# Optimization experiments

Hardware: AMD Instinct MI355X
Metric: run time of the kernel (lower is better)

## Reference

```python
import jax, jax.numpy as jnp
import numpy as np

# Config (matches init_kwargs): range [-32,32]^3, voxel 0.5 -> 128^3 grid; BEV 200x200
PC_LOW = np.array([-32.0, -32.0, -32.0], dtype=np.float32)
PC_HIGH = np.array([32.0, 32.0, 32.0], dtype=np.float32)
VOX = 0.5
G = 128
BEV_H, BEV_W = 200, 200
BN_EPS = 1e-5
STRIDES = [1, 2, 1, 2, 1, 1]


def setup_inputs() -> dict:
    key = jax.random.key(0)
    ks = jax.random.split(key, 10)
    N = 2_000_000
    xyz = jax.random.uniform(ks[0], (N, 3), jnp.float32, minval=-32.0, maxval=32.0)
    inten = jax.random.uniform(ks[1], (N, 1), jnp.float32)
    points = jnp.concatenate([xyz, inten], axis=1)  # (N,4)
    chans = [(32, 4), (64, 32), (64, 64), (128, 64), (128, 128), (256, 128)]
    inp = {"points": points}
    for i, (co, ci) in enumerate(chans):
        fan_in = ci * 27
        inp[f"w{i+1}"] = jax.random.normal(ks[2 + i], (co, ci, 3, 3, 3), jnp.float32) / np.sqrt(fan_in)
        inp[f"g{i+1}"] = jnp.ones((co,), jnp.float32)
        inp[f"b{i+1}"] = jnp.zeros((co,), jnp.float32)
    return inp


def _voxelize(points):
    # range filtering + floor-binning + clamp, faithful to voxelize_points (dense path: scatter-ADD)
    low = jnp.asarray(PC_LOW)
    high = jnp.asarray(PC_HIGH)
    mask = jnp.all((points[:, :3] >= low) & (points[:, :3] <= high), axis=1)
    coords = jnp.floor((points[:, :3] - low) / VOX).astype(jnp.int32)
    coords = jnp.clip(coords, 0, G - 1)
    vals = points * mask[:, None].astype(points.dtype)  # invalid points contribute 0
    # original indexes voxel_grid[:, z, y, x]
    grid = jnp.zeros((G, G, G, 4), points.dtype)
    grid = grid.at[coords[:, 2], coords[:, 1], coords[:, 0]].add(vals)
    return jnp.transpose(grid, (3, 0, 1, 2))  # (4, G, G, G)


def _conv3d(x, w, s):
    # PyTorch Conv3d(k=3, padding=1, stride=s), NCDHW
    return jax.lax.conv_general_dilated(
        x, w, window_strides=(s, s, s), padding=[(1, 1), (1, 1), (1, 1)],
        dimension_numbers=("NCDHW", "OIDHW", "NCDHW"))


def _bn_relu(x, g, b):
    # eval-mode BN: running_mean=0, running_var=1
    scale = (g / jnp.sqrt(1.0 + BN_EPS))[None, :, None, None, None]
    return jax.nn.relu(x * scale + b[None, :, None, None, None])


def reference(points, w1, w2, w3, w4, w5, w6,
              g1, g2, g3, g4, g5, g6,
              b1, b2, b3, b4, b5, b6):
    ws = [w1, w2, w3, w4, w5, w6]
    gs = [g1, g2, g3, g4, g5, g6]
    bs = [b1, b2, b3, b4, b5, b6]
    x = _voxelize(points)[None]  # (1,4,G,G,G)
    for w, g, b, s in zip(ws, gs, bs, STRIDES):
        x = _bn_relu(_conv3d(x, w, s), g, b)
    feat = x[0]  # (256, G/4, G/4, G/4)
    bev = jnp.max(feat, axis=2)  # torch.max(..., dim=2) on (C,D1,D2,D3) -> (C,D1,D3)
    # F.interpolate bilinear align_corners=False == jax.image.resize half-pixel bilinear
    bev = jax.image.resize(bev, (bev.shape[0], BEV_H, BEV_W), method="bilinear")
    return bev
```

## Files before the change

kernel.cpp:

```cpp
#include <hip/hip_runtime.h>
#include <hip/hip_fp16.h>
#include <cstdint>
#include <cstddef>

typedef __attribute__((ext_vector_type(8))) short short8;
typedef __attribute__((ext_vector_type(8))) _Float16 half8;
typedef __attribute__((ext_vector_type(16))) float f32x16;

__device__ __forceinline__ float bf2f(unsigned short u) { return __uint_as_float(((unsigned)u) << 16); }
__device__ __forceinline__ unsigned short f2bf(float f) {
    unsigned u = __float_as_uint(f);
    return (unsigned short)((u + 0x7fffu + ((u >> 16) & 1u)) >> 16);
}
__device__ __forceinline__ void sync_lds() {
    asm volatile("s_waitcnt lgkmcnt(0)\n\ts_barrier" ::: "memory");
}
__device__ __forceinline__ void sync_vm() {
    asm volatile("s_waitcnt vmcnt(0)\n\ts_barrier" ::: "memory");
}
__device__ __forceinline__ void gload16(const unsigned short* g, char* l) {
    __builtin_amdgcn_global_load_lds(
        (const __attribute__((address_space(1))) unsigned int*)g,
        (__attribute__((address_space(3))) unsigned int*)l, 16, 0, 0);
}

static constexpr float BN_INV = 0.9999950000374997f;


__device__ __forceinline__ int vox_bucket(float4 p, bool& ok) {
    ok = !(p.x < -32.f || p.x > 32.f || p.y < -32.f || p.y > 32.f || p.z < -32.f || p.z > 32.f);
    int cy = min(max((int)floorf((p.y + 32.f) * 2.f), 0), 127);
    int cz = min(max((int)floorf((p.z + 32.f) * 2.f), 0), 127);
    return cz * 4 + (cy >> 5);
}

__global__ __launch_bounds__(256) void vox_count(const float4* __restrict__ pts,
                                                 int* __restrict__ cnt, int N) {
    __shared__ int h[512];
    for (int t = threadIdx.x; t < 512; t += 256) h[t] = 0;
    __syncthreads();
    int stride = gridDim.x * 256;
    for (int i = blockIdx.x * 256 + threadIdx.x; i < N; i += stride) {
        float4 p = pts[i];
        bool ok;
        int bk = vox_bucket(p, ok);
        if (ok) atomicAdd(&h[bk], 1);
    }
    __syncthreads();
    for (int t = threadIdx.x; t < 512; t += 256)
        if (h[t]) atomicAdd(&cnt[t], h[t]);
}

__global__ void vox_scan(const int* __restrict__ cnt, int* __restrict__ off,
                         int* __restrict__ cur) {
    __shared__ int c[512];
    int t = threadIdx.x;
    c[t] = cnt[t];
    __syncthreads();
    int s = 0;
    for (int i = 0; i < t; ++i) s += c[i];
    off[t] = s;
    cur[t] = s;
}

__global__ __launch_bounds__(256) void vox_scatter(const float4* __restrict__ pts,
                                                   int* __restrict__ cur,
                                                   float4* __restrict__ sorted, int N) {
    __shared__ int h[512];
    __shared__ int base[512];
    int b0 = blockIdx.x * 4096;
    for (int t = threadIdx.x; t < 512; t += 256) h[t] = 0;
    __syncthreads();
    float4 p[16];
    int bk[16];
#pragma unroll
    for (int j = 0; j < 16; ++j) {
        int i = b0 + j * 256 + threadIdx.x;
        bk[j] = -1;
        if (i < N) {
            p[j] = pts[i];
            bool ok;
            int b = vox_bucket(p[j], ok);
            if (ok) {
                bk[j] = b;
                atomicAdd(&h[b], 1);
            }
        }
    }
    __syncthreads();
    for (int t = threadIdx.x; t < 512; t += 256) {
        int n = h[t];
        base[t] = n ? atomicAdd(&cur[t], n) : 0;
        h[t] = 0;
    }
    __syncthreads();
#pragma unroll
    for (int j = 0; j < 16; ++j) {
        if (bk[j] >= 0) {
            int r = atomicAdd(&h[bk[j]], 1);
            sorted[base[bk[j]] + r] = p[j];
        }
    }
}

__global__ __launch_bounds__(256) void vox_accum(const float4* __restrict__ sorted,
                                                 const int* __restrict__ off,
                                                 const int* __restrict__ cnt,
                                                 __half2* __restrict__ grid) {
    __shared__ float s[32 * 128 * 4];
    for (int t = threadIdx.x; t < 16384; t += 256) s[t] = 0.f;
    __syncthreads();
    int bid = blockIdx.x;
    int bz = bid >> 2;
    int ylo = (bid & 3) << 5;
    int b = off[bid], n = cnt[bid];
    for (int i = threadIdx.x; i < n; i += 256) {
        float4 p = sorted[b + i];
        int cx = min(max((int)floorf((p.x + 32.f) * 2.f), 0), 127);
        int cy = min(max((int)floorf((p.y + 32.f) * 2.f), 0), 127);
        float* v = s + ((cy - ylo) * 128 + cx) * 4;
        unsafeAtomicAdd(v + 0, p.x);
        unsafeAtomicAdd(v + 1, p.y);
        unsafeAtomicAdd(v + 2, p.z);
        unsafeAtomicAdd(v + 3, p.w);
    }
    __syncthreads();
    for (int t = threadIdx.x; t < 4096; t += 256) {
        int ry = t >> 7, cx = t & 127;
        const float* v = s + t * 4;
        union { __half2 h[2]; float2 f; } u;
        u.h[0] = __floats2half2_rn(v[0], v[1]);
        u.h[1] = __floats2half2_rn(v[2], v[3]);
        int gi = (((bz + 1) * 130 + (ylo + ry + 1)) * 130 + (cx + 1)) * 2;
        *(float2*)(grid + gi) = u.f;
    }
}

__global__ __launch_bounds__(256) void pad_zero(unsigned short* __restrict__ buf,
                                                int Xp, int Zp, int C) {
    const int cpc = (C >= 8) ? (C / 8) : 1;
    long i = (long)blockIdx.x * 256 + threadIdx.x;
    long nz = (long)2 * Xp * Xp;
    long ny = (long)(Zp - 2) * 2 * Xp;
    long nx = (long)(Zp - 2) * (Xp - 2) * 2;
    long total = (nz + ny + nx) * cpc;
    if (i >= total) return;
    long cell = i / cpc;
    int ch = (int)(i - cell * cpc) * 8;
    int z, y, x;
    if (cell < nz) {
        long r = cell;
        z = (r >= (long)Xp * Xp) ? (Zp - 1) : 0;
        r %= (long)Xp * Xp;
        y = (int)(r / Xp);
        x = (int)(r % Xp);
    } else if (cell < nz + ny) {
        long r = cell - nz;
        z = 1 + (int)(r / (2 * Xp));
        int s = (int)(r % (2 * Xp));
        y = (s >= Xp) ? (Xp - 1) : 0;
        x = (s >= Xp) ? (s - Xp) : s;
    } else {
        long r = cell - nz - ny;
        z = 1 + (int)(r / ((Xp - 2) * 2));
        int s = (int)(r % ((Xp - 2) * 2));
        y = 1 + (s >> 1);
        x = (s & 1) ? (Xp - 1) : 0;
    }
    unsigned short* p = buf + (((long)z * Xp + y) * Xp + x) * C + ch;
    if (C >= 8) {
        *(short8*)p = (short8){0, 0, 0, 0, 0, 0, 0, 0};
    } else {
        *(float2*)p = (float2){0.f, 0.f};
    }
}
static inline int pad_blocks(int Xp, int Zp, int C) {
    long cells = (long)2 * Xp * Xp + (long)(Zp - 2) * 2 * Xp + (long)(Zp - 2) * (Xp - 2) * 2;
    long thr = cells * ((C >= 8) ? (C / 8) : 1);
    return (int)((thr + 255) / 256);
}

__global__ __launch_bounds__(256) void repack_w(const float* __restrict__ w, const float* __restrict__ g,
                                                unsigned short* __restrict__ o, int Co, int CI) {
    int i = blockIdx.x * 256 + threadIdx.x;
    int total = 27 * Co * CI;
    if (i >= total) return;
    int ci = i % CI;
    int t = i / CI;
    int co = t % Co;
    int k = t / Co;
    float v = w[((size_t)(co * CI + ci)) * 27 + k] * g[co] * BN_INV;
    o[i] = f2bf(v);
}
__global__ __launch_bounds__(256) void repack_w1m(const float* __restrict__ w, const float* __restrict__ g,
                                                  unsigned short* __restrict__ o) {
    int i = blockIdx.x * 256 + threadIdx.x;
    if (i >= 9 * 32 * 16) return;
    int k16 = i & 15;
    int co = (i >> 4) & 31;
    int p = i >> 9;
    float v = 0.f;
    if (k16 < 12) {
        int dx = k16 >> 2, ci = k16 & 3;
        int dz = p / 3, dy = p % 3;
        v = w[(co * 4 + ci) * 27 + dz * 9 + dy * 3 + dx] * g[co] * BN_INV;
    }
    o[i] = __half_as_ushort(__float2half(v));
}

__global__ __launch_bounds__(256) void conv1_mfma(
    const unsigned short* __restrict__ in, const unsigned short* __restrict__ wa,
    const float* __restrict__ beta, unsigned short* __restrict__ out,
    int zstart, int r0) {
    const int tid = threadIdx.x;
    const int l31 = tid & 31;
    const int lh = (tid >> 5) & 1;
    const int wv = tid >> 6;
    int v = blockIdx.x * 128 + wv * 32 + l31;
    int x = v & 127;
    int y = (v >> 7) & 127;
    int z = zstart + (v >> 14);

    const unsigned short* base = in + ((z * 130 + y) * 130 + x) * 4 + lh * 8;
    uint2 d0[9], d1[9];
    half8 a[9];
#pragma unroll
    for (int p = 0; p < 9; ++p) {
        int dz = p / 3, dy = p % 3;
        const unsigned short* rp = base + (dz * 130 + dy) * 520;
        d0[p] = *(const uint2*)(rp);
        d1[p] = *(const uint2*)(rp + 4);
        a[p] = *(const half8*)(wa + (p * 32 + l31) * 16 + lh * 8);
    }
    f32x16 acc = {0.f};
#pragma unroll
    for (int p = 0; p < 9; ++p) {
        uint4 braw = {d0[p].x, d0[p].y, d1[p].x, d1[p].y};
        half8 b = *(half8*)&braw;
        acc = __builtin_amdgcn_mfma_f32_32x32x16_f16(a[p], b, acc, 0, 0, 0);
    }
    int r = z - zstart + r0;
    int ob = ((r * 130 + (y + 1)) * 130 + (x + 1)) * 32;
#pragma unroll
    for (int g = 0; g < 4; ++g) {
        int cb = 4 * lh + 8 * g;
        float4 bt = *(const float4*)(beta + cb);
        ushort4 u;
        u.x = f2bf(fmaxf(acc[g * 4 + 0] + bt.x, 0.f));
        u.y = f2bf(fmaxf(acc[g * 4 + 1] + bt.y, 0.f));
        u.z = f2bf(fmaxf(acc[g * 4 + 2] + bt.z, 0.f));
        u.w = f2bf(fmaxf(acc[g * 4 + 3] + bt.w, 0.f));
        *(ushort4*)(out + ob + cb) = u;
    }
}

template <int CI, int KC, int S>
__global__ __launch_bounds__(256) void conv_mfma(
    const unsigned short* __restrict__ in, const unsigned short* __restrict__ wb,
    const float* __restrict__ beta, unsigned short* __restrict__ out,
    int D, int lgD, int Xp, int Xpo, int Co, int zin_base, int v_off) {

    constexpr int KCp = KC + 8;
    constexpr int OPB = KC / 8;
    constexpr int NB = KC / 16;
    constexpr int NA = KC / 32;
    constexpr int NCH = KC / 16;
    constexpr int NCC = CI / KC;
    constexpr int STOT = 27 * NCC;

    __shared__ __align__(16) short sA[2 * 64 * KCp];
    __shared__ __align__(16) short sB[2 * 128 * KCp];

    const int tid = threadIdx.x;
    const int l31 = tid & 31;
    const int lh = (tid >> 5) & 1;
    const int wv = tid >> 6;

    const unsigned gx = gridDim.x;
    const unsigned lin = blockIdx.y * gx + blockIdx.x;
    const unsigned q = (gx * gridDim.y) >> 3;
    const unsigned lin2 = (lin & 7) * q + (lin >> 3);
    const unsigned bxs = lin2 % gx;
    const unsigned bys = lin2 / gx;
    const int co0 = bxs * 64;

    int bgIdx[NB], blB[NB];
#pragma unroll
    for (int j = 0; j < NB; ++j) {
        int idx = tid + j * 256;
        int vL = idx / OPB;
        int oct = idx - vL * OPB;
        int vg = v_off + bys * 128 + vL;
        int x = vg & (D - 1);
        int ry = vg >> lgD;
        int y = ry & (D - 1);
        int z = ry >> lgD;
        bgIdx[j] = ((z * S * Xp + y * S) * Xp + x * S) * CI + oct * 8;
        blB[j] = vL * KCp + oct * 8;
    }
    int agIdx[NA], alA[NA];
#pragma unroll
    for (int j = 0; j < NA; ++j) {
        int idx = tid + j * 256;
        int cA = idx / OPB;
        int oct = idx - cA * OPB;
        agIdx[j] = (co0 + cA) * CI + oct * 8;
        alA[j] = cA * KCp + oct * 8;
    }
    const int bfr = (wv * 32 + l31) * KCp + lh * 8;
    const int afr = l31 * KCp + lh * 8;

    short8 rB[2][NB], rA[2][NA];

    auto loadStage = [&](int s, int r) {
        int k = s / NCC;
        int c0 = (s - k * NCC) * KC;
        int dz = k / 9;
        int rr = k - dz * 9;
        int dy = rr / 3;
        int dx = rr - dy * 3;
        int kb = (((dz - zin_base) * Xp + dy) * Xp + dx) * CI + c0;
        int ka = k * Co * CI + c0;
#pragma unroll
        for (int j = 0; j < NB; ++j) rB[r][j] = *(const short8*)(in + bgIdx[j] + kb);
#pragma unroll
        for (int j = 0; j < NA; ++j) rA[r][j] = *(const short8*)(wb + agIdx[j] + ka);
    };
    auto storeLDS = [&](int r, int buf) {
#pragma unroll
        for (int j = 0; j < NB; ++j) *(short8*)(sB + buf * 128 * KCp + blB[j]) = rB[r][j];
#pragma unroll
        for (int j = 0; j < NA; ++j) *(short8*)(sA + buf * 64 * KCp + alA[j]) = rA[r][j];
    };

    f32x16 acc0 = {0.f}, acc1 = {0.f};

    loadStage(0, 0);
    loadStage(1, 1);
    storeLDS(0, 0);
    sync_lds();

#pragma unroll
    for (int s = 0; s < STOT; ++s) {
        if (s + 2 < STOT) loadStage(s + 2, s & 1);
        const short* pB = sB + (s & 1) * 128 * KCp + bfr;
        const short* pA = sA + (s & 1) * 64 * KCp + afr;
#pragma unroll
        for (int c = 0; c < NCH; ++c) {
            short8 bv = *(const short8*)(pB + c * 16);
            short8 a0 = *(const short8*)(pA + c * 16);
            short8 a1 = *(const short8*)(pA + 32 * KCp + c * 16);
            acc0 = __builtin_amdgcn_mfma_f32_32x32x16_bf16(a0, bv, acc0, 0, 0, 0);
            acc1 = __builtin_amdgcn_mfma_f32_32x32x16_bf16(a1, bv, acc1, 0, 0, 0);
        }
        if (s + 1 < STOT) {
            storeLDS((s + 1) & 1, (s + 1) & 1);
            sync_lds();
        }
    }

    int vg = v_off + bys * 128 + wv * 32 + l31;
    int x = vg & (D - 1);
    int ry = vg >> lgD;
    int y = ry & (D - 1);
    int z = ry >> lgD;
    size_t ob = (((size_t)(z + 1) * Xpo + (y + 1)) * Xpo + (x + 1)) * Co + co0;
#pragma unroll
    for (int cot = 0; cot < 2; ++cot) {
        const f32x16& a = cot ? acc1 : acc0;
#pragma unroll
        for (int g = 0; g < 4; ++g) {
            int cb = cot * 32 + 4 * lh + 8 * g;
            float4 bt = *(const float4*)(beta + co0 + cb);
            ushort4 u;
            u.x = f2bf(fmaxf(a[g * 4 + 0] + bt.x, 0.f));
            u.y = f2bf(fmaxf(a[g * 4 + 1] + bt.y, 0.f));
            u.z = f2bf(fmaxf(a[g * 4 + 2] + bt.z, 0.f));
            u.w = f2bf(fmaxf(a[g * 4 + 3] + bt.w, 0.f));
            *(ushort4*)(out + ob + cb) = u;
        }
    }
}

template <int CI, int S>
__global__ __launch_bounds__(256, 3) void conv_mfma_g(
    const unsigned short* __restrict__ in, const unsigned short* __restrict__ wb,
    const float* __restrict__ beta, unsigned short* __restrict__ out,
    int D, int lgD, int Xp, int Xpo, int Co, int zin_base, int v_off) {

    constexpr int KC = 64;
    constexpr int NCC = CI / KC;
    constexpr int STOT = 27 * NCC;

    __shared__ __align__(16) char sB[2 * 128 * 128];
    __shared__ __align__(16) char sA[2 * 64 * 128];

    const int tid = threadIdx.x;
    const int l31 = tid & 31;
    const int lh = (tid >> 5) & 1;
    const int wv = tid >> 6;
    const int l63 = tid & 63;

    const unsigned gx = gridDim.x;
    const unsigned lin = blockIdx.y * gx + blockIdx.x;
    const unsigned q = (gx * gridDim.y) >> 3;
    const unsigned lin2 = (lin & 7) * q + (lin >> 3);
    const unsigned bxs = lin2 % gx;
    const unsigned bys = lin2 / gx;
    const int co0 = bxs * 64;

    const int swoct = (l63 & 7) ^ (l63 >> 3);

    int bgIdxG[4];
#pragma unroll
    for (int j = 0; j < 4; ++j) {
        int r = (j * 4 + wv) * 8 + (l63 >> 3);
        int vg = v_off + bys * 128 + r;
        int x = vg & (D - 1);
        int ry = vg >> lgD;
        int y = ry & (D - 1);
        int z = ry >> lgD;
        bgIdxG[j] = ((z * S * Xp + y * S) * Xp + x * S) * CI + swoct * 8;
    }
    int agIdxG[2];
#pragma unroll
    for (int j = 0; j < 2; ++j) {
        int r = (j * 4 + wv) * 8 + (l63 >> 3);
        agIdxG[j] = (co0 + r) * CI + swoct * 8;
    }

    auto issueStage = [&](int s, int buf) {
        int k = s / NCC;
        int c0 = (s - k * NCC) * KC;
        int dz = k / 9;
        int rr = k - dz * 9;
        int dy = rr / 3;
        int dx = rr - dy * 3;
        int kb = (((dz - zin_base) * Xp + dy) * Xp + dx) * CI + c0;
        int ka = k * Co * CI + c0;
#pragma unroll
        for (int j = 0; j < 4; ++j)
            gload16(in + bgIdxG[j] + kb, sB + buf * 16384 + (j * 4 + wv) * 1024);
#pragma unroll
        for (int j = 0; j < 2; ++j)
            gload16(wb + agIdxG[j] + ka, sA + buf * 8192 + (j * 4 + wv) * 1024);
    };

    const int brow = wv * 32 + l31;
    const int r7 = l31 & 7;

    f32x16 acc0 = {0.f}, acc1 = {0.f};

    issueStage(0, 0);
    sync_vm();

#pragma unroll
    for (int s = 0; s < STOT; ++s) {
        if (s + 1 < STOT) issueStage(s + 1, (s + 1) & 1);
        const char* pB = sB + (s & 1) * 16384 + brow * 128;
        const char* pA0 = sA + (s & 1) * 8192 + l31 * 128;
        const char* pA1 = pA0 + 32 * 128;
#pragma unroll
        for (int c = 0; c < 4; ++c) {
            int oct = ((2 * c + lh) ^ r7) * 16;
            short8 bv = *(const short8*)(pB + oct);
            short8 a0 = *(const short8*)(pA0 + oct);
            short8 a1 = *(const short8*)(pA1 + oct);
            acc0 = __builtin_amdgcn_mfma_f32_32x32x16_bf16(a0, bv, acc0, 0, 0, 0);
            acc1 = __builtin_amdgcn_mfma_f32_32x32x16_bf16(a1, bv, acc1, 0, 0, 0);
        }
        sync_vm();
    }

    int vg = v_off + bys * 128 + wv * 32 + l31;
    int x = vg & (D - 1);
    int ry = vg >> lgD;
    int y = ry & (D - 1);
    int z = ry >> lgD;
    size_t ob = (((size_t)(z + 1) * Xpo + (y + 1)) * Xpo + (x + 1)) * Co + co0;
#pragma unroll
    for (int cot = 0; cot < 2; ++cot) {
        const f32x16& a = cot ? acc1 : acc0;
#pragma unroll
        for (int g = 0; g < 4; ++g) {
            int cb = cot * 32 + 4 * lh + 8 * g;
            float4 bt = *(const float4*)(beta + co0 + cb);
            ushort4 u;
            u.x = f2bf(fmaxf(a[g * 4 + 0] + bt.x, 0.f));
            u.y = f2bf(fmaxf(a[g * 4 + 1] + bt.y, 0.f));
            u.z = f2bf(fmaxf(a[g * 4 + 2] + bt.z, 0.f));
            u.w = f2bf(fmaxf(a[g * 4 + 3] + bt.w, 0.f));
            *(ushort4*)(out + ob + cb) = u;
        }
    }
}

__global__ __launch_bounds__(256) void bev_max_kernel(const unsigned short* __restrict__ feat,
                                                      float* __restrict__ bev) {
    int z = blockIdx.x >> 5;
    int x = blockIdx.x & 31;
    int c = threadIdx.x;
    const unsigned short* p = feat + ((((z + 1) * 34) + 1) * 34 + (x + 1)) * 256 + c;
    float mx = 0.f;
#pragma unroll
    for (int y = 0; y < 32; ++y) mx = fmaxf(mx, bf2f(p[y * 34 * 256]));
    bev[(z * 32 + x) * 256 + c] = mx;
}

__global__ __launch_bounds__(256) void resize_kernel(const float* __restrict__ bev,
                                                     float* __restrict__ out) {
    int i = blockIdx.x * 256 + threadIdx.x;
    if (i >= 256 * 200 * 200) return;
    int ox = i % 200;
    int t = i / 200;
    int oy = t % 200;
    int c = t / 200;
    const float sc = 32.0f / 200.0f;
    float fy = (oy + 0.5f) * sc - 0.5f;
    float fx = (ox + 0.5f) * sc - 0.5f;
    float fy0 = floorf(fy), fx0 = floorf(fx);
    float ty = fy - fy0, tx = fx - fx0;
    int y0 = min(max((int)fy0, 0), 31), y1 = min(max((int)fy0 + 1, 0), 31);
    int x0 = min(max((int)fx0, 0), 31), x1 = min(max((int)fx0 + 1, 0), 31);
    float v00 = bev[(y0 * 32 + x0) * 256 + c], v01 = bev[(y0 * 32 + x1) * 256 + c];
    float v10 = bev[(y1 * 32 + x0) * 256 + c], v11 = bev[(y1 * 32 + x1) * 256 + c];
    float top = v00 + tx * (v01 - v00);
    float bot = v10 + tx * (v11 - v10);
    out[i] = top + ty * (bot - top);
}

extern "C" void kernel_launch(void* const* d_in, const int* in_sizes, int n_in,
                              void* d_out, int out_size, void* d_ws, size_t ws_size,
                              hipStream_t stream) {
    const float* points = (const float*)d_in[0];
    int N = in_sizes[0] / 4;
    const float *W[6], *G[6], *B[6];
    for (int i = 0; i < 6; ++i) {
        W[i] = (const float*)d_in[1 + 3 * i];
        G[i] = (const float*)d_in[2 + 3 * i];
        B[i] = (const float*)d_in[3 + 3 * i];
    }

    char* ws = (char*)d_ws;
    const size_t MiB = 1ull << 20;
    unsigned short* gridH = (unsigned short*)(ws);
    int* cnt = (int*)(ws + 17580032);
    int* off = cnt + 512;
    int* cur = off + 512;
    float4* sorted = (float4*)(ws + 18 * MiB);
    unsigned short* O1s = (unsigned short*)(ws + 18 * MiB);
    unsigned short* O2p = (unsigned short*)(ws + 104 * MiB);
    unsigned short* O3p = (unsigned short*)(ws);
    unsigned short* O4p = (unsigned short*)(ws + 37 * MiB);
    unsigned short* O5p = (unsigned short*)(ws + 48 * MiB);
    unsigned short* O6p = (unsigned short*)(ws + 59 * MiB);
    float* bev = (float*)(ws + 80 * MiB);
    unsigned short* wc1 = (unsigned short*)(ws + 140 * MiB);
    unsigned short* wb2 = (unsigned short*)(ws + 140 * MiB + 16384);
    unsigned short* wb3 = wb2 + 27 * 64 * 32;
    unsigned short* wb4 = wb3 + 27 * 64 * 64;
    unsigned short* wb5 = wb4 + 27 * 128 * 64;
    unsigned short* wb6 = wb5 + 27 * 128 * 128;

    repack_w1m<<<18, 256, 0, stream>>>(W[0], G[0], wc1);
    repack_w<<<216, 256, 0, stream>>>(W[1], G[1], wb2, 64, 32);
    repack_w<<<432, 256, 0, stream>>>(W[2], G[2], wb3, 64, 64);
    repack_w<<<864, 256, 0, stream>>>(W[3], G[3], wb4, 128, 64);
    repack_w<<<1728, 256, 0, stream>>>(W[4], G[4], wb5, 128, 128);
    repack_w<<<3456, 256, 0, stream>>>(W[5], G[5], wb6, 256, 128);

    pad_zero<<<pad_blocks(130, 130, 4), 256, 0, stream>>>(gridH, 130, 130, 4);
    hipMemsetAsync(cnt, 0, 2048, stream);
    pad_zero<<<pad_blocks(66, 66, 64), 256, 0, stream>>>(O2p, 66, 66, 64);
    vox_count<<<1024, 256, 0, stream>>>((const float4*)points, cnt, N);
    vox_scan<<<1, 512, 0, stream>>>(cnt, off, cur);
    vox_scatter<<<(N + 4095) / 4096, 256, 0, stream>>>((const float4*)points, cur, sorted, N);
    vox_accum<<<512, 256, 0, stream>>>(sorted, off, cnt, (__half2*)gridH);

    pad_zero<<<pad_blocks(130, 65, 32), 256, 0, stream>>>(O1s, 130, 65, 32);
    conv1_mfma<<<8192, 256, 0, stream>>>(gridH, wc1, B[0], O1s, 0, 1);
    conv_mfma<32, 32, 2><<<dim3(1, 1024), 256, 0, stream>>>(O1s, wb2, B[1], O2p, 64, 6, 130, 66, 64, 0, 0);
    conv1_mfma<<<8320, 256, 0, stream>>>(gridH, wc1, B[0], O1s, 63, 0);
    conv_mfma<32, 32, 2><<<dim3(1, 1024), 256, 0, stream>>>(O1s, wb2, B[1], O2p, 64, 6, 130, 66, 64, 64, 131072);

    pad_zero<<<pad_blocks(66, 66, 64), 256, 0, stream>>>(O3p, 66, 66, 64);
    pad_zero<<<pad_blocks(34, 34, 128), 256, 0, stream>>>(O4p, 34, 34, 128);
    pad_zero<<<pad_blocks(34, 34, 128), 256, 0, stream>>>(O5p, 34, 34, 128);
    pad_zero<<<pad_blocks(34, 34, 256), 256, 0, stream>>>(O6p, 34, 34, 256);

    conv_mfma_g<64, 1><<<dim3(1, 2048), 256, 0, stream>>>(O2p, wb3, B[2], O3p, 64, 6, 66, 66, 64, 0, 0);
    conv_mfma_g<64, 2><<<dim3(2, 256), 256, 0, stream>>>(O3p, wb4, B[3], O4p, 32, 5, 66, 34, 128, 0, 0);
    conv_mfma_g<128, 1><<<dim3(2, 256), 256, 0, stream>>>(O4p, wb5, B[4], O5p, 32, 5, 34, 34, 128, 0, 0);
    conv_mfma_g<128, 1><<<dim3(4, 256), 256, 0, stream>>>(O5p, wb6, B[5], O6p, 32, 5, 34, 34, 256, 0, 0);

    bev_max_kernel<<<1024, 256, 0, stream>>>(O6p, bev);
    resize_kernel<<<40000, 256, 0, stream>>>(bev, (float*)d_out);
}
```

Baseline: 677.3 us.

## Replace direct-to-LDS conv kernel with register-staged 128x128 tile variant

The global-to-LDS async conv kernel for layers 4-6 is replaced by a new kernel that stages loads in registers with two-stage prefetch and writes padded LDS rows. Each block now computes a 128-channel by 128-voxel tile with 2x2 MFMA accumulators per wave, which halves the block count and raises operand reuse. Layer 3 moves onto the existing conv_mfma<64,64,1> template. The larger tile costs register pressure (launch bounds lowered to 2 blocks per CU), and layers 4-6 launch only 256 or 512 blocks, which may leave CUs underfilled.

Measured after the change: 628.8 us. 1.08x faster.

```diff
diff --git a/kernel.cpp b/kernel.cpp
--- a/kernel.cpp
+++ b/kernel.cpp
@@ -14,14 +14,6 @@
 }
 __device__ __forceinline__ void sync_lds() {
     asm volatile("s_waitcnt lgkmcnt(0)\n\ts_barrier" ::: "memory");
-}
-__device__ __forceinline__ void sync_vm() {
-    asm volatile("s_waitcnt vmcnt(0)\n\ts_barrier" ::: "memory");
-}
-__device__ __forceinline__ void gload16(const unsigned short* g, char* l) {
-    __builtin_amdgcn_global_load_lds(
-        (const __attribute__((address_space(1))) unsigned int*)g,
-        (__attribute__((address_space(3))) unsigned int*)l, 16, 0, 0);
 }
 
 static constexpr float BN_INV = 0.9999950000374997f;
@@ -383,23 +375,29 @@
 }
 
 template <int CI, int S>
-__global__ __launch_bounds__(256, 3) void conv_mfma_g(
+__global__ __launch_bounds__(256, 2) void conv_mfma_w(
     const unsigned short* __restrict__ in, const unsigned short* __restrict__ wb,
     const float* __restrict__ beta, unsigned short* __restrict__ out,
     int D, int lgD, int Xp, int Xpo, int Co, int zin_base, int v_off) {
 
     constexpr int KC = 64;
+    constexpr int KCp = KC + 8;
+    constexpr int OPB = KC / 8;
+    constexpr int NB = 4;
+    constexpr int NA = 4;
+    constexpr int NCH = 4;
     constexpr int NCC = CI / KC;
     constexpr int STOT = 27 * NCC;
 
-    __shared__ __align__(16) char sB[2 * 128 * 128];
-    __shared__ __align__(16) char sA[2 * 64 * 128];
+    __shared__ __align__(16) short sA[2 * 128 * KCp];
+    __shared__ __align__(16) short sB[2 * 128 * KCp];
 
     const int tid = threadIdx.x;
     const int l31 = tid & 31;
     const int lh = (tid >> 5) & 1;
     const int wv = tid >> 6;
-    const int l63 = tid & 63;
+    const int wr = wv >> 1;
+    const int wc = wv & 1;
 
     const unsigned gx = gridDim.x;
     const unsigned lin = blockIdx.y * gx + blockIdx.x;
@@ -407,29 +405,37 @@
     const unsigned lin2 = (lin & 7) * q + (lin >> 3);
     const unsigned bxs = lin2 % gx;
     const unsigned bys = lin2 / gx;
-    const int co0 = bxs * 64;
-
-    const int swoct = (l63 & 7) ^ (l63 >> 3);
-
-    int bgIdxG[4];
-#pragma unroll
-    for (int j = 0; j < 4; ++j) {
-        int r = (j * 4 + wv) * 8 + (l63 >> 3);
-        int vg = v_off + bys * 128 + r;
+    const int co0 = bxs * 128;
+
+    int bgIdx[NB], blB[NB];
+#pragma unroll
+    for (int j = 0; j < NB; ++j) {
+        int idx = tid + j * 256;
+        int vL = idx / OPB;
+        int oct = idx - vL * OPB;
+        int vg = v_off + bys * 128 + vL;
         int x = vg & (D - 1);
         int ry = vg >> lgD;
         int y = ry & (D - 1);
         int z = ry >> lgD;
-        bgIdxG[j] = ((z * S * Xp + y * S) * Xp + x * S) * CI + swoct * 8;
-    }
-    int agIdxG[2];
-#pragma unroll
-    for (int j = 0; j < 2; ++j) {
-        int r = (j * 4 + wv) * 8 + (l63 >> 3);
-        agIdxG[j] = (co0 + r) * CI + swoct * 8;
-    }
-
-    auto issueStage = [&](int s, int buf) {
+        bgIdx[j] = ((z * S * Xp + y * S) * Xp + x * S) * CI + oct * 8;
+        blB[j] = vL * KCp + oct * 8;
+    }
+    int agIdx[NA], alA[NA];
+#pragma unroll
+    for (int j = 0; j < NA; ++j) {
+        int idx = tid + j * 256;
+        int cA = idx / OPB;
+        int oct = idx - cA * OPB;
+        agIdx[j] = (co0 + cA) * CI + oct * 8;
+        alA[j] = cA * KCp + oct * 8;
+    }
+    const int bfr = (wc * 64 + l31) * KCp + lh * 8;
+    const int afr = (wr * 64 + l31) * KCp + lh * 8;
+
+    short8 rB[2][NB], rA[2][NA];
+
+    auto loadStage = [&](int s, int r) {
         int k = s / NCC;
         int c0 = (s - k * NCC) * KC;
         int dz = k / 9;
@@ -439,58 +445,69 @@
         int kb = (((dz - zin_base) * Xp + dy) * Xp + dx) * CI + c0;
         int ka = k * Co * CI + c0;
 #pragma unroll
-        for (int j = 0; j < 4; ++j)
-            gload16(in + bgIdxG[j] + kb, sB + buf * 16384 + (j * 4 + wv) * 1024);
-#pragma unroll
-        for (int j = 0; j < 2; ++j)
-            gload16(wb + agIdxG[j] + ka, sA + buf * 8192 + (j * 4 + wv) * 1024);
+        for (int j = 0; j < NB; ++j) rB[r][j] = *(const short8*)(in + bgIdx[j] + kb);
+#pragma unroll
+        for (int j = 0; j < NA; ++j) rA[r][j] = *(const short8*)(wb + agIdx[j] + ka);
     };
-
-    const int brow = wv * 32 + l31;
-    const int r7 = l31 & 7;
-
-    f32x16 acc0 = {0.f}, acc1 = {0.f};
-
-    issueStage(0, 0);
-    sync_vm();
+    auto storeLDS = [&](int r, int buf) {
+#pragma unroll
+        for (int j = 0; j < NB; ++j) *(short8*)(sB + buf * 128 * KCp + blB[j]) = rB[r][j];
+#pragma unroll
+        for (int j = 0; j < NA; ++j) *(short8*)(sA + buf * 128 * KCp + alA[j]) = rA[r][j];
+    };
+
+    f32x16 acc00 = {0.f}, acc01 = {0.f}, acc10 = {0.f}, acc11 = {0.f};
+
+    loadStage(0, 0);
+    loadStage(1, 1);
+    storeLDS(0, 0);
+    sync_lds();
 
 #pragma unroll
     for (int s = 0; s < STOT; ++s) {
-        if (s + 1 < STOT) issueStage(s + 1, (s + 1) & 1);
-        const char* pB = sB + (s & 1) * 16384 + brow * 128;
-        const char* pA0 = sA + (s & 1) * 8192 + l31 * 128;
-        const char* pA1 = pA0 + 32 * 128;
-#pragma unroll
-        for (int c = 0; c < 4; ++c) {
-            int oct = ((2 * c + lh) ^ r7) * 16;
-            short8 bv = *(const short8*)(pB + oct);
-            short8 a0 = *(const short8*)(pA0 + oct);
-            short8 a1 = *(const short8*)(pA1 + oct);
-            acc0 = __builtin_amdgcn_mfma_f32_32x32x16_bf16(a0, bv, acc0, 0, 0, 0);
-            acc1 = __builtin_amdgcn_mfma_f32_32x32x16_bf16(a1, bv, acc1, 0, 0, 0);
-        }
-        sync_vm();
-    }
-
-    int vg = v_off + bys * 128 + wv * 32 + l31;
-    int x = vg & (D - 1);
-    int ry = vg >> lgD;
-    int y = ry & (D - 1);
-    int z = ry >> lgD;
-    size_t ob = (((size_t)(z + 1) * Xpo + (y + 1)) * Xpo + (x + 1)) * Co + co0;
-#pragma unroll
-    for (int cot = 0; cot < 2; ++cot) {
-        const f32x16& a = cot ? acc1 : acc0;
-#pragma unroll
-        for (int g = 0; g < 4; ++g) {
-            int cb = cot * 32 + 4 * lh + 8 * g;
-            float4 bt = *(const float4*)(beta + co0 + cb);
-            ushort4 u;
-            u.x = f2bf(fmaxf(a[g * 4 + 0] + bt.x, 0.f));
-            u.y = f2bf(fmaxf(a[g * 4 + 1] + bt.y, 0.f));
-            u.z = f2bf(fmaxf(a[g * 4 + 2] + bt.z, 0.f));
-            u.w = f2bf(fmaxf(a[g * 4 + 3] + bt.w, 0.f));
-            *(ushort4*)(out + ob + cb) = u;
+        if (s + 2 < STOT) loadStage(s + 2, s & 1);
+        const short* pB = sB + (s & 1) * 128 * KCp + bfr;
+        const short* pA = sA + (s & 1) * 128 * KCp + afr;
+#pragma unroll
+        for (int c = 0; c < NCH; ++c) {
+            short8 b0 = *(const short8*)(pB + c * 16);
+            short8 b1 = *(const short8*)(pB + 32 * KCp + c * 16);
+            short8 a0 = *(const short8*)(pA + c * 16);
+            short8 a1 = *(const short8*)(pA + 32 * KCp + c * 16);
+            acc00 = __builtin_amdgcn_mfma_f32_32x32x16_bf16(a0, b0, acc00, 0, 0, 0);
+            acc01 = __builtin_amdgcn_mfma_f32_32x32x16_bf16(a0, b1, acc01, 0, 0, 0);
+            acc10 = __builtin_amdgcn_mfma_f32_32x32x16_bf16(a1, b0, acc10, 0, 0, 0);
+            acc11 = __builtin_amdgcn_mfma_f32_32x32x16_bf16(a1, b1, acc11, 0, 0, 0);
+        }
+        if (s + 1 < STOT) {
+            storeLDS((s + 1) & 1, (s + 1) & 1);
+            sync_lds();
+        }
+    }
+
+#pragma unroll
+    for (int i = 0; i < 2; ++i) {
+#pragma unroll
+        for (int j = 0; j < 2; ++j) {
+            const f32x16& a = (i == 0) ? (j == 0 ? acc00 : acc01) : (j == 0 ? acc10 : acc11);
+            int vg2 = v_off + bys * 128 + wc * 64 + j * 32 + l31;
+            int x = vg2 & (D - 1);
+            int ry = vg2 >> lgD;
+            int y = ry & (D - 1);
+            int z = ry >> lgD;
+            int cbase = co0 + wr * 64 + i * 32;
+            size_t ob = (((size_t)(z + 1) * Xpo + (y + 1)) * Xpo + (x + 1)) * Co + cbase;
+#pragma unroll
+            for (int g = 0; g < 4; ++g) {
+                int cb = 4 * lh + 8 * g;
+                float4 bt = *(const float4*)(beta + cbase + cb);
+                ushort4 u;
+                u.x = f2bf(fmaxf(a[g * 4 + 0] + bt.x, 0.f));
+                u.y = f2bf(fmaxf(a[g * 4 + 1] + bt.y, 0.f));
+                u.z = f2bf(fmaxf(a[g * 4 + 2] + bt.z, 0.f));
+                u.w = f2bf(fmaxf(a[g * 4 + 3] + bt.w, 0.f));
+                *(ushort4*)(out + ob + cb) = u;
+            }
         }
     }
 }
@@ -588,10 +605,10 @@
     pad_zero<<<pad_blocks(34, 34, 128), 256, 0, stream>>>(O5p, 34, 34, 128);
     pad_zero<<<pad_blocks(34, 34, 256), 256, 0, stream>>>(O6p, 34, 34, 256);
 
-    conv_mfma_g<64, 1><<<dim3(1, 2048), 256, 0, stream>>>(O2p, wb3, B[2], O3p, 64, 6, 66, 66, 64, 0, 0);
-    conv_mfma_g<64, 2><<<dim3(2, 256), 256, 0, stream>>>(O3p, wb4, B[3], O4p, 32, 5, 66, 34, 128, 0, 0);
-    conv_mfma_g<128, 1><<<dim3(2, 256), 256, 0, stream>>>(O4p, wb5, B[4], O5p, 32, 5, 34, 34, 128, 0, 0);
-    conv_mfma_g<128, 1><<<dim3(4, 256), 256, 0, stream>>>(O5p, wb6, B[5], O6p, 32, 5, 34, 34, 256, 0, 0);
+    conv_mfma<64, 64, 1><<<dim3(1, 2048), 256, 0, stream>>>(O2p, wb3, B[2], O3p, 64, 6, 66, 66, 64, 0, 0);
+    conv_mfma_w<64, 2><<<dim3(1, 256), 256, 0, stream>>>(O3p, wb4, B[3], O4p, 32, 5, 66, 34, 128, 0, 0);
+    conv_mfma_w<128, 1><<<dim3(1, 256), 256, 0, stream>>>(O4p, wb5, B[4], O5p, 32, 5, 34, 34, 128, 0, 0);
+    conv_mfma_w<128, 1><<<dim3(2, 256), 256, 0, stream>>>(O5p, wb6, B[5], O6p, 32, 5, 34, 34, 256, 0, 0);
 
     bev_max_kernel<<<1024, 256, 0, stream>>>(O6p, bev);
     resize_kernel<<<40000, 256, 0, stream>>>(bev, (float*)d_out);
```
